# Optimization experiments

Hardware: AMD Instinct MI355X
Metric: run time of the kernel (lower is better)

The kernel has to match this reference:

```python
import jax, jax.numpy as jnp
import numpy as np
from functools import reduce

N_QUBITS = 12
DIM = 2 ** N_QUBITS          # 4096 state-vector dimension
DEPTH = 6                    # ansatz rotation layers
BATCH = 256
OBSERVE_BITS = (0, 1, 2)     # Pauli-Z expectation on these qubits
INPUT_SCALING = np.pi


def setup_inputs() -> dict:
    key = jax.random.key(0)
    k1, k2 = jax.random.split(key)
    input_tensor = jax.random.uniform(k1, (BATCH, N_QUBITS), dtype=jnp.float32)
    # param_init_range = (-pi/depth, pi/depth)
    thetas = jax.random.normal(k2, (DEPTH, N_QUBITS), dtype=jnp.float32) * (np.pi / DEPTH)
    return {"input_tensor": input_tensor, "thetas": thetas}


def _ry(theta):
    # RY(theta) = [[cos t/2, -sin t/2], [sin t/2, cos t/2]]
    h = theta * 0.5
    c, s = jnp.cos(h), jnp.sin(h)
    return jnp.stack([jnp.stack([c, -s]), jnp.stack([s, c])]).astype(jnp.complex64)


def _cnot_ladder_perm():
    # CNOT(i -> i+1) for i = 0..n-2; each CNOT is a basis permutation that
    # flips the target bit when the control bit is 1. Compose permutations
    # (applied in reverse order so state_out = state_in[perm]). Qubit 0 is the
    # leftmost kron factor, i.e. bit position n-1-q of the basis index.
    perm = np.arange(DIM)
    for cq, tq in reversed([(i, i + 1) for i in range(N_QUBITS - 1)]):
        cbit, tbit = N_QUBITS - 1 - cq, N_QUBITS - 1 - tq
        flip = ((perm >> cbit) & 1) == 1
        perm = np.where(flip, perm ^ (1 << tbit), perm)
    return jnp.asarray(perm)


_PERM = _cnot_ladder_perm()


def _forward(input_tensor, thetas):
    # --- encoder: RY(pi * x_q) applied to |0...0> gives a product state ---
    half = input_tensor * (INPUT_SCALING * 0.5)          # [B, n] half-angles
    c, s = jnp.cos(half), jnp.sin(half)
    psi = jnp.ones((BATCH, 1), dtype=jnp.complex64)
    for q in range(N_QUBITS):                            # fixed small loop over qubits
        amp = jnp.stack([c[:, q], s[:, q]], axis=-1).astype(jnp.complex64)  # [B, 2]
        psi = (psi[:, :, None] * amp[:, None, :]).reshape(BATCH, -1)
    state = psi.T                                        # [DIM, B] complex64

    # --- ansatz: per-depth full-unitary (kron of per-qubit gates) mm, then CNOT ladder ---
    for d in range(DEPTH):
        U = reduce(jnp.kron, [_ry(thetas[d, q]) for q in range(N_QUBITS)])  # [DIM, DIM]
        state = U @ state                                # Hamiltonian @ state (torch.mm)
        state = state[_PERM]                             # entangling CNOT ladder

    # --- observer: <Z_q> on each observed qubit ---
    probs = state.real ** 2 + state.imag ** 2            # [DIM, B]
    idx = jnp.arange(DIM)
    zdiag = jnp.stack([1.0 - 2.0 * ((idx >> (N_QUBITS - 1 - q)) & 1)
                       for q in OBSERVE_BITS]).astype(jnp.float32)          # [K, DIM]
    return jnp.einsum('kn,nb->bk', zdiag, probs)         # [B, K]


def reference(input_tensor, thetas):
    return _forward(input_tensor, thetas)
```

## Files before the change

kernel.cpp:

```cpp
#include <hip/hip_runtime.h>
#include <math.h>
#include <type_traits>

#define NQ     12
#define DIM    4096
#define DEPTH  6
#define NBATCH 256
#define NT     256
#define NREG   16


__host__ __device__ constexpr unsigned axmask(int d, int b) {
    unsigned m = 1u << b;
    for (int i = 0; i < d; ++i) m = (m ^ (m >> 1)) & 0xFFFu;
    return m;
}
__host__ __device__ constexpr unsigned selmask(int d, int b) {
    unsigned m = 1u << b;
    for (int i = 0; i < 16 - d; ++i) m = (m ^ ((m << 1) & 0xFFFu)) & 0xFFFu;
    return m;
}
__host__ __device__ constexpr int cpopc(unsigned v) {
    int c = 0; while (v) { c += (int)(v & 1u); v >>= 1; } return c;
}

template<int I, int N, class F>
__device__ __forceinline__ void sfor(F&& f) {
    if constexpr (I < N) {
        f(std::integral_constant<int, I>{});
        sfor<I + 1, N>(static_cast<F&&>(f));
    }
}

template<int MASK>
__device__ __forceinline__ float lxor(float v) {
    static_assert(MASK > 0 && MASK < 64, "lane mask");
    if constexpr (MASK == 1 || MASK == 2 || MASK == 3 || MASK == 7 || MASK == 15) {
        constexpr int ctrl = (MASK == 1) ? 0xB1
                           : (MASK == 2) ? 0x4E
                           : (MASK == 3) ? 0x1B
                           : (MASK == 7) ? 0x141
                           :               0x140;
        int iv = __float_as_int(v);
        return __int_as_float(__builtin_amdgcn_update_dpp(iv, iv, ctrl, 0xF, 0xF, false));
    } else if constexpr (MASK < 32) {
        return __int_as_float(__builtin_amdgcn_ds_swizzle(__float_as_int(v),
                                                          (MASK << 10) | 0x1F));
    } else {
        return __shfl_xor(v, MASK, 64);
    }
}

template<int D, int B>
__device__ __forceinline__ void gate_reg(float (&st)[NREG], const int tid,
                                         float c, float s) {
    constexpr unsigned V = axmask(D, B), M = selmask(D, B);
    constexpr int VR = (int)(V & 15u);
    static_assert((V >> 4) == 0, "reg gate");
    constexpr unsigned MR = M & 15u, MT = M >> 4;
    const float sp = (__popc(MT & (unsigned)tid) & 1) ? s : -s;
    sfor<0, NREG>([&](auto RC) {
        constexpr int r = RC.value, r2 = r ^ VR;
        if constexpr (r2 > r) {
            constexpr bool p0 = (cpopc(MR & (unsigned)r)  & 1) != 0;
            constexpr bool p1 = (cpopc(MR & (unsigned)r2) & 1) != 0;
            float a0 = st[r], a1 = st[r2];
            float t0 = sp * a1, t1 = sp * a0;
            st[r]  = fmaf(c, a0, p0 ? -t0 : t0);
            st[r2] = fmaf(c, a1, p1 ? -t1 : t1);
        }
    });
}

template<int D, int B>
__device__ __forceinline__ void gate_shfl(float (&st)[NREG], const int tid,
                                          float c, float s) {
    constexpr unsigned V = axmask(D, B), M = selmask(D, B);
    constexpr int VT = (int)(V >> 4), VR = (int)(V & 15u);
    static_assert(VT > 0 && (VT >> 6) == 0, "intra-wave gate");
    static_assert((M & 15u) == 0, "mask has no reg bits for b>=4");
    const float sp = (__popc((M >> 4) & (unsigned)tid) & 1) ? s : -s;
    if constexpr (VR == 0) {
        sfor<0, NREG>([&](auto RC) {
            constexpr int r = RC.value;
            float p = lxor<VT>(st[r]);
            st[r] = fmaf(c, st[r], sp * p);
        });
    } else {
        sfor<0, NREG>([&](auto RC) {
            constexpr int r = RC.value, r2 = r ^ VR;
            if constexpr (r2 > r) {
                float pa = lxor<VT>(st[r2]);
                float pb = lxor<VT>(st[r]);
                st[r]  = fmaf(c, st[r],  sp * pa);
                st[r2] = fmaf(c, st[r2], sp * pb);
            }
        });
    }
}

template<int D>
__device__ __forceinline__ void cross2(float (&st)[NREG], const int tid,
                                       float2 cs1, float2 cs2,
                                       float* __restrict__ lds) {
    constexpr unsigned V1 = axmask(D, 11), V2 = axmask(D, 10);
    constexpr unsigned M1 = selmask(D, 11), M2 = selmask(D, 10);
    static_assert((V1 & 15u) == 0 && (V2 & 15u) == 0, "cross axes thread-pure");
    static_assert((M1 & 15u) == 0 && (M2 & 15u) == 0, "cross masks thread-pure");
    constexpr int T1 = (int)(V1 >> 4), T2 = (int)(V2 >> 4);
    static_assert((cpopc(M1 & V2) & 1) == 0, "kC sign identity");

    const float e1 = (__popc((M1 >> 4) & (unsigned)tid) & 1) ? 1.f : -1.f;
    const float e2 = (__popc((M2 >> 4) & (unsigned)tid) & 1) ? 1.f : -1.f;
    const float k0 = cs1.x * cs2.x;
    const float kA = cs1.y * cs2.x * e1;
    const float kB = cs1.x * cs2.y * e2;
    const float kC = cs1.y * cs2.y * e1 * e2;

    float* buf = lds + (D & 1) * DIM;
    const int sw = tid & 3;
    sfor<0, 4>([&](auto KC) {
        constexpr int k = KC.value;
        *reinterpret_cast<float4*>(&buf[tid * 16 + 4 * (k ^ sw)]) =
            make_float4(st[4*k], st[4*k+1], st[4*k+2], st[4*k+3]);
    });
    __syncthreads();
    const int p1 = tid ^ T1, p2 = tid ^ T2, p3 = tid ^ (T1 ^ T2);
    const int b1 = p1 * 16, s1w = p1 & 3;
    const int b2 = p2 * 16, s2w = p2 & 3;
    const int b3 = p3 * 16, s3w = p3 & 3;
    sfor<0, 4>([&](auto KC) {
        constexpr int k = KC.value;
        float4 A  = *reinterpret_cast<const float4*>(&buf[b1 + 4 * (k ^ s1w)]);
        float4 Bv = *reinterpret_cast<const float4*>(&buf[b2 + 4 * (k ^ s2w)]);
        float4 Cv = *reinterpret_cast<const float4*>(&buf[b3 + 4 * (k ^ s3w)]);
        float t;
        t = k0 * st[4*k+0]; t = fmaf(kA, A.x, t); t = fmaf(kB, Bv.x, t); st[4*k+0] = fmaf(kC, Cv.x, t);
        t = k0 * st[4*k+1]; t = fmaf(kA, A.y, t); t = fmaf(kB, Bv.y, t); st[4*k+1] = fmaf(kC, Cv.y, t);
        t = k0 * st[4*k+2]; t = fmaf(kA, A.z, t); t = fmaf(kB, Bv.z, t); st[4*k+2] = fmaf(kC, Cv.z, t);
        t = k0 * st[4*k+3]; t = fmaf(kA, A.w, t); t = fmaf(kB, Bv.w, t); st[4*k+3] = fmaf(kC, Cv.w, t);
    });
}

template<int D>
__device__ __forceinline__ void depth_apply(float (&st)[NREG], const int tid,
                                            const float2* __restrict__ gcs2,
                                            float* __restrict__ lds) {
    float2 cs[12];
    sfor<0, 12>([&](auto QC) { cs[QC.value] = gcs2[D * 12 + QC.value]; });
    cross2<D>(st, tid, cs[0], cs[1], lds);
    sfor<2, 12>([&](auto QC) {
        constexpr int Q = QC.value, B = 11 - Q;
        if constexpr (B >= 4) gate_shfl<D, B>(st, tid, cs[Q].x, cs[Q].y);
        else                  gate_reg <D, B>(st, tid, cs[Q].x, cs[Q].y);
    });
}

__global__ __launch_bounds__(NT, 1)
void qnet_kernel(const float* __restrict__ x,
                 const float* __restrict__ thetas,
                 float* __restrict__ out)
{
    __shared__ __align__(16) float lds[2 * DIM];
    __shared__ float2 gcs2[72];
    __shared__ float red[12];

    const int b   = blockIdx.x;
    const int tid = threadIdx.x;

    if (tid < 72) {
        float rev = thetas[tid] * 0.07957747154594767f;
        gcs2[tid] = make_float2(__builtin_amdgcn_cosf(rev),
                                __builtin_amdgcn_sinf(rev));
    }

    const float4* xv = reinterpret_cast<const float4*>(x + b * 12);
    float4 xa = xv[0], xb = xv[1], xc = xv[2];
    float xs[12] = {xa.x, xa.y, xa.z, xa.w, xb.x, xb.y, xb.z, xb.w,
                    xc.x, xc.y, xc.z, xc.w};
    float cq[12], sq[12];
    sfor<0, 12>([&](auto QC) {
        constexpr int q = QC.value;
        float rev = xs[q] * 0.25f;
        sq[q] = __builtin_amdgcn_sinf(rev);
        cq[q] = __builtin_amdgcn_cosf(rev);
    });

    float la = 1.0f;
    sfor<0, 8>([&](auto IC) {
        constexpr int i = IC.value;
        la *= ((tid >> i) & 1) ? sq[7 - i] : cq[7 - i];
    });

    float st[NREG];
    st[0] = la;
    sfor<0, 4>([&](auto IC) {
        constexpr int i = IC.value;
        sfor<0, (1 << i)>([&](auto KC) {
            constexpr int k = KC.value;
            float base = st[k];
            st[k + (1 << i)] = base * sq[11 - i];
            st[k]            = base * cq[11 - i];
        });
    });

    __syncthreads();

    sfor<0, 6>([&](auto DC) { depth_apply<DC.value>(st, tid, gcs2, lds); });

    float tot = 0.0f;
    sfor<0, NREG>([&](auto RC) {
        constexpr int r = RC.value;
        tot = fmaf(st[r], st[r], tot);
    });

    float a0 = ((tid >> 7) & 1)                ? -tot : tot;
    float a1 = ((tid >> 6) & 1)                ? -tot : tot;
    float a2 = (((tid >> 7) ^ (tid >> 5)) & 1) ? -tot : tot;

    #pragma unroll
    for (int off = 32; off; off >>= 1) {
        a0 += __shfl_xor(a0, off, 64);
        a1 += __shfl_xor(a1, off, 64);
        a2 += __shfl_xor(a2, off, 64);
    }
    const int lane = tid & 63, w = tid >> 6;
    if (lane == 0) {
        red[w * 3 + 0] = a0;
        red[w * 3 + 1] = a1;
        red[w * 3 + 2] = a2;
    }
    __syncthreads();
    if (tid < 3)
        out[b * 3 + tid] = red[tid] + red[3 + tid] + red[6 + tid] + red[9 + tid];
}

extern "C" void kernel_launch(void* const* d_in, const int* in_sizes, int n_in,
                              void* d_out, int out_size, void* d_ws, size_t ws_size,
                              hipStream_t stream) {
    (void)in_sizes; (void)n_in; (void)out_size; (void)d_ws; (void)ws_size;
    const float* x      = (const float*)d_in[0];
    const float* thetas = (const float*)d_in[1];
    float* out          = (float*)d_out;

    qnet_kernel<<<dim3(NBATCH), dim3(NT), 0, stream>>>(x, thetas, out);
}
```

Measured before the change: 16.06 us.

## Factor cosines out of rotation gates, use tangent form and DPP-only reductions

Each RY gate is rewritten as cos times a [[1,-tan],[tan,1]] shear, so every gate update becomes a single FMA. The product of cosines is accumulated and applied once to the final probabilities. Per-thread theta trig replaces the shared-memory table and its barrier, and the lane xor for masks below 16 is composed from DPP row ops. The final reduction is restructured into one butterfly plus a sign split. The tangent form can lose accuracy or blow up if a cosine approaches zero, and every thread now recomputes 72 sin/cos pairs.

```diff
diff --git a/kernel.cpp b/kernel.cpp
--- a/kernel.cpp
+++ b/kernel.cpp
@@ -32,59 +32,69 @@
     }
 }
 
+template<int CTRL>
+__device__ __forceinline__ float dppx(float v) {
+    int iv = __float_as_int(v);
+    return __int_as_float(__builtin_amdgcn_update_dpp(iv, iv, CTRL, 0xF, 0xF, false));
+}
+template<int M4>
+__device__ __forceinline__ float lxor_low(float v) {
+    static_assert(M4 >= 1 && M4 <= 15, "low mask");
+    if constexpr      (M4 == 1)  return dppx<0xB1>(v);
+    else if constexpr (M4 == 2)  return dppx<0x4E>(v);
+    else if constexpr (M4 == 3)  return dppx<0x1B>(v);
+    else if constexpr (M4 == 7)  return dppx<0x141>(v);
+    else if constexpr (M4 == 15) return dppx<0x140>(v);
+    else if constexpr ((M4 & 8) == 0)
+        return lxor_low<M4 ^ 7>(dppx<0x141>(v));
+    else
+        return lxor_low<M4 ^ 15>(dppx<0x140>(v));
+}
 template<int MASK>
 __device__ __forceinline__ float lxor(float v) {
     static_assert(MASK > 0 && MASK < 64, "lane mask");
-    if constexpr (MASK == 1 || MASK == 2 || MASK == 3 || MASK == 7 || MASK == 15) {
-        constexpr int ctrl = (MASK == 1) ? 0xB1
-                           : (MASK == 2) ? 0x4E
-                           : (MASK == 3) ? 0x1B
-                           : (MASK == 7) ? 0x141
-                           :               0x140;
-        int iv = __float_as_int(v);
-        return __int_as_float(__builtin_amdgcn_update_dpp(iv, iv, ctrl, 0xF, 0xF, false));
-    } else if constexpr (MASK < 32) {
+    if constexpr (MASK >= 32) {
+        return __shfl_xor(v, MASK, 64);
+    } else if constexpr (MASK >= 16) {
         return __int_as_float(__builtin_amdgcn_ds_swizzle(__float_as_int(v),
                                                           (MASK << 10) | 0x1F));
     } else {
-        return __shfl_xor(v, MASK, 64);
+        return lxor_low<MASK>(v);
     }
 }
 
 template<int D, int B>
-__device__ __forceinline__ void gate_reg(float (&st)[NREG], const int tid,
-                                         float c, float s) {
+__device__ __forceinline__ void gate_reg(float (&st)[NREG], int tid, float t) {
     constexpr unsigned V = axmask(D, B), M = selmask(D, B);
-    constexpr int VR = (int)(V & 15u);
-    static_assert((V >> 4) == 0, "reg gate");
+    static_assert((V >> 4) == 0 && V != 0, "reg gate");
+    constexpr int VR = (int)V;
     constexpr unsigned MR = M & 15u, MT = M >> 4;
-    const float sp = (__popc(MT & (unsigned)tid) & 1) ? s : -s;
+    const float tp = (__popc(MT & (unsigned)tid) & 1) ? t : -t;
+    const float tn = -tp;
     sfor<0, NREG>([&](auto RC) {
         constexpr int r = RC.value, r2 = r ^ VR;
         if constexpr (r2 > r) {
             constexpr bool p0 = (cpopc(MR & (unsigned)r)  & 1) != 0;
             constexpr bool p1 = (cpopc(MR & (unsigned)r2) & 1) != 0;
-            float a0 = st[r], a1 = st[r2];
-            float t0 = sp * a1, t1 = sp * a0;
-            st[r]  = fmaf(c, a0, p0 ? -t0 : t0);
-            st[r2] = fmaf(c, a1, p1 ? -t1 : t1);
+            float a0 = st[r];
+            st[r]  = fmaf(p0 ? tn : tp, st[r2], st[r]);
+            st[r2] = fmaf(p1 ? tn : tp, a0,     st[r2]);
         }
     });
 }
 
 template<int D, int B>
-__device__ __forceinline__ void gate_shfl(float (&st)[NREG], const int tid,
-                                          float c, float s) {
+__device__ __forceinline__ void gate_lane(float (&st)[NREG], int tid, float t) {
     constexpr unsigned V = axmask(D, B), M = selmask(D, B);
     constexpr int VT = (int)(V >> 4), VR = (int)(V & 15u);
-    static_assert(VT > 0 && (VT >> 6) == 0, "intra-wave gate");
-    static_assert((M & 15u) == 0, "mask has no reg bits for b>=4");
-    const float sp = (__popc((M >> 4) & (unsigned)tid) & 1) ? s : -s;
+    static_assert(VT > 0 && VT < 64, "intra-wave gate");
+    static_assert((M & 15u) == 0, "no reg bits in selector for b>=4");
+    const float tp = (__popc((M >> 4) & (unsigned)tid) & 1) ? t : -t;
     if constexpr (VR == 0) {
         sfor<0, NREG>([&](auto RC) {
             constexpr int r = RC.value;
             float p = lxor<VT>(st[r]);
-            st[r] = fmaf(c, st[r], sp * p);
+            st[r] = fmaf(tp, p, st[r]);
         });
     } else {
         sfor<0, NREG>([&](auto RC) {
@@ -92,16 +102,16 @@
             if constexpr (r2 > r) {
                 float pa = lxor<VT>(st[r2]);
                 float pb = lxor<VT>(st[r]);
-                st[r]  = fmaf(c, st[r],  sp * pa);
-                st[r2] = fmaf(c, st[r2], sp * pb);
+                st[r]  = fmaf(tp, pa, st[r]);
+                st[r2] = fmaf(tp, pb, st[r2]);
             }
         });
     }
 }
 
 template<int D>
-__device__ __forceinline__ void cross2(float (&st)[NREG], const int tid,
-                                       float2 cs1, float2 cs2,
+__device__ __forceinline__ void cross2(float (&st)[NREG], int tid,
+                                       float t1, float t2,
                                        float* __restrict__ lds) {
     constexpr unsigned V1 = axmask(D, 11), V2 = axmask(D, 10);
     constexpr unsigned M1 = selmask(D, 11), M2 = selmask(D, 10);
@@ -110,12 +120,9 @@
     constexpr int T1 = (int)(V1 >> 4), T2 = (int)(V2 >> 4);
     static_assert((cpopc(M1 & V2) & 1) == 0, "kC sign identity");
 
-    const float e1 = (__popc((M1 >> 4) & (unsigned)tid) & 1) ? 1.f : -1.f;
-    const float e2 = (__popc((M2 >> 4) & (unsigned)tid) & 1) ? 1.f : -1.f;
-    const float k0 = cs1.x * cs2.x;
-    const float kA = cs1.y * cs2.x * e1;
-    const float kB = cs1.x * cs2.y * e2;
-    const float kC = cs1.y * cs2.y * e1 * e2;
+    const float t1p = (__popc((M1 >> 4) & (unsigned)tid) & 1) ? t1 : -t1;
+    const float t2p = (__popc((M2 >> 4) & (unsigned)tid) & 1) ? t2 : -t2;
+    const float t12 = t1p * t2p;
 
     float* buf = lds + (D & 1) * DIM;
     const int sw = tid & 3;
@@ -135,25 +142,34 @@
         float4 Bv = *reinterpret_cast<const float4*>(&buf[b2 + 4 * (k ^ s2w)]);
         float4 Cv = *reinterpret_cast<const float4*>(&buf[b3 + 4 * (k ^ s3w)]);
         float t;
-        t = k0 * st[4*k+0]; t = fmaf(kA, A.x, t); t = fmaf(kB, Bv.x, t); st[4*k+0] = fmaf(kC, Cv.x, t);
-        t = k0 * st[4*k+1]; t = fmaf(kA, A.y, t); t = fmaf(kB, Bv.y, t); st[4*k+1] = fmaf(kC, Cv.y, t);
-        t = k0 * st[4*k+2]; t = fmaf(kA, A.z, t); t = fmaf(kB, Bv.z, t); st[4*k+2] = fmaf(kC, Cv.z, t);
-        t = k0 * st[4*k+3]; t = fmaf(kA, A.w, t); t = fmaf(kB, Bv.w, t); st[4*k+3] = fmaf(kC, Cv.w, t);
+        t = fmaf(t1p, A.x, st[4*k+0]); t = fmaf(t2p, Bv.x, t); st[4*k+0] = fmaf(t12, Cv.x, t);
+        t = fmaf(t1p, A.y, st[4*k+1]); t = fmaf(t2p, Bv.y, t); st[4*k+1] = fmaf(t12, Cv.y, t);
+        t = fmaf(t1p, A.z, st[4*k+2]); t = fmaf(t2p, Bv.z, t); st[4*k+2] = fmaf(t12, Cv.z, t);
+        t = fmaf(t1p, A.w, st[4*k+3]); t = fmaf(t2p, Bv.w, t); st[4*k+3] = fmaf(t12, Cv.w, t);
     });
 }
 
 template<int D>
-__device__ __forceinline__ void depth_apply(float (&st)[NREG], const int tid,
-                                            const float2* __restrict__ gcs2,
-                                            float* __restrict__ lds) {
-    float2 cs[12];
-    sfor<0, 12>([&](auto QC) { cs[QC.value] = gcs2[D * 12 + QC.value]; });
-    cross2<D>(st, tid, cs[0], cs[1], lds);
+__device__ __forceinline__ float depth_apply(float (&st)[NREG], int tid,
+                                             const float* __restrict__ thetas,
+                                             float* __restrict__ lds) {
+    float tq[12];
+    float scd = 1.0f;
+    sfor<0, 12>([&](auto QC) {
+        constexpr int q = QC.value;
+        float rev = thetas[D * 12 + q] * 0.07957747154594767f;
+        float cc  = __builtin_amdgcn_cosf(rev);
+        float ss  = __builtin_amdgcn_sinf(rev);
+        tq[q] = ss * __builtin_amdgcn_rcpf(cc);
+        scd  *= cc;
+    });
+    cross2<D>(st, tid, tq[0], tq[1], lds);
     sfor<2, 12>([&](auto QC) {
         constexpr int Q = QC.value, B = 11 - Q;
-        if constexpr (B >= 4) gate_shfl<D, B>(st, tid, cs[Q].x, cs[Q].y);
-        else                  gate_reg <D, B>(st, tid, cs[Q].x, cs[Q].y);
-    });
+        if constexpr (B >= 4) gate_lane<D, B>(st, tid, tq[Q]);
+        else                  gate_reg <D, B>(st, tid, tq[Q]);
+    });
+    return scd;
 }
 
 __global__ __launch_bounds__(NT, 1)
@@ -162,17 +178,10 @@
                  float* __restrict__ out)
 {
     __shared__ __align__(16) float lds[2 * DIM];
-    __shared__ float2 gcs2[72];
-    __shared__ float red[12];
+    __shared__ float red[8];
 
     const int b   = blockIdx.x;
     const int tid = threadIdx.x;
-
-    if (tid < 72) {
-        float rev = thetas[tid] * 0.07957747154594767f;
-        gcs2[tid] = make_float2(__builtin_amdgcn_cosf(rev),
-                                __builtin_amdgcn_sinf(rev));
-    }
 
     const float4* xv = reinterpret_cast<const float4*>(x + b * 12);
     float4 xa = xv[0], xb = xv[1], xc = xv[2];
@@ -191,7 +200,6 @@
         constexpr int i = IC.value;
         la *= ((tid >> i) & 1) ? sq[7 - i] : cq[7 - i];
     });
-
     float st[NREG];
     st[0] = la;
     sfor<0, 4>([&](auto IC) {
@@ -204,35 +212,34 @@
         });
     });
 
-    __syncthreads();
-
-    sfor<0, 6>([&](auto DC) { depth_apply<DC.value>(st, tid, gcs2, lds); });
+    float sc = 1.0f;
+    sfor<0, 6>([&](auto DC) {
+        sc *= depth_apply<DC.value>(st, tid, thetas, lds);
+    });
 
     float tot = 0.0f;
     sfor<0, NREG>([&](auto RC) {
         constexpr int r = RC.value;
         tot = fmaf(st[r], st[r], tot);
     });
-
-    float a0 = ((tid >> 7) & 1)                ? -tot : tot;
-    float a1 = ((tid >> 6) & 1)                ? -tot : tot;
-    float a2 = (((tid >> 7) ^ (tid >> 5)) & 1) ? -tot : tot;
-
-    #pragma unroll
-    for (int off = 32; off; off >>= 1) {
-        a0 += __shfl_xor(a0, off, 64);
-        a1 += __shfl_xor(a1, off, 64);
-        a2 += __shfl_xor(a2, off, 64);
-    }
-    const int lane = tid & 63, w = tid >> 6;
-    if (lane == 0) {
-        red[w * 3 + 0] = a0;
-        red[w * 3 + 1] = a1;
-        red[w * 3 + 2] = a2;
+    tot *= sc * sc;
+
+    float v = tot;
+    v += lxor<1>(v);
+    v += lxor<2>(v);
+    v += lxor<4>(v);
+    v += lxor<8>(v);
+    v += lxor<16>(v);
+    float u = lxor<32>(v);
+    const int w = tid >> 6;
+    if ((tid & 63) == 0) {
+        red[w]     = v + u;
+        red[4 + w] = v - u;
     }
     __syncthreads();
-    if (tid < 3)
-        out[b * 3 + tid] = red[tid] + red[3 + tid] + red[6 + tid] + red[9 + tid];
+    if (tid == 0) out[b * 3 + 0] = (red[0] + red[1]) - (red[2] + red[3]);
+    if (tid == 1) out[b * 3 + 1] = (red[0] - red[1]) + (red[2] - red[3]);
+    if (tid == 2) out[b * 3 + 2] = (red[4] + red[5]) - (red[6] + red[7]);
 }
 
 extern "C" void kernel_launch(void* const* d_in, const int* in_sizes, int n_in,
```

New measurement: 15.70 us. 1.02x faster.
